# Optimization experiments

Measured on AMD Instinct MI355X. Metric: run time of the kernel, lower is better.

## Reference

```python
import jax, jax.numpy as jnp
import numpy as np

B, K, N, D, L = 16, 16, 1024, 256, 8
LN_EPS = 1e-5


def setup_inputs() -> dict:
    key = jax.random.key(0)
    ks = jax.random.split(key, 12)
    w = lambda k, sh: jax.random.normal(k, sh, jnp.float32) * 0.02
    return {
        "H": jax.random.normal(ks[0], (B, K, N, D), jnp.float32),
        "eps": jax.random.normal(ks[1], (B, L, D), jnp.float32),  # single Gaussian draw per batch
        "mu": jnp.zeros((1, L, D), jnp.float32),
        "log_sigma": jnp.full((1, L, D), -2.0, jnp.float32),
        "Wq": w(ks[2], (D, D)), "bq": jnp.zeros((D,), jnp.float32),
        "Wk": w(ks[3], (D, D)), "bk": jnp.zeros((D,), jnp.float32),
        "Wv": w(ks[4], (D, D)), "bv": jnp.zeros((D,), jnp.float32),
        "W_ih": w(ks[5], (3 * D, D)), "b_ih": jnp.zeros((3 * D,), jnp.float32),
        "W_hh": w(ks[6], (3 * D, D)), "b_hh": jnp.zeros((3 * D,), jnp.float32),
        "W1": w(ks[7], (D, D)), "b1": jnp.zeros((D,), jnp.float32),
        "W2": w(ks[8], (D, D)), "b2": jnp.zeros((D,), jnp.float32),
        "ln_g": jnp.ones((D,), jnp.float32), "ln_b": jnp.zeros((D,), jnp.float32),
    }


def reference(H, eps, mu, log_sigma, Wq, bq, Wk, bk, Wv, bv,
              W_ih, b_ih, W_hh, b_hh, W1, b1, W2, b2, ln_g, ln_b):
    d = H.shape[-1]
    scale = 1.0 / jnp.sqrt(jnp.asarray(d, H.dtype))
    slots0 = mu + jnp.exp(log_sigma) * eps  # [B,L,D]

    def step(slots, h_t):  # slots [B,L,D], h_t [B,N,D]
        Q = slots @ Wq.T + bq
        Kt = h_t @ Wk.T + bk
        V = h_t @ Wv.T + bv
        scores = jnp.einsum("bld,bnd->bln", Q, Kt) * scale
        attn = jnp.nan_to_num(jax.nn.softmax(scores, axis=-1))
        upd = jnp.einsum("bln,bnd->bld", attn, V)
        # torch.nn.GRUCell(input=upd, hidden=slots)
        gi = upd @ W_ih.T + b_ih
        gh = slots @ W_hh.T + b_hh
        ir, iz, inn = jnp.split(gi, 3, axis=-1)
        hr, hz, hn = jnp.split(gh, 3, axis=-1)
        r = jax.nn.sigmoid(ir + hr)
        z = jax.nn.sigmoid(iz + hz)
        n = jnp.tanh(inn + r * hn)
        s2 = (1.0 - z) * n + z * slots
        # FFN + residual + LayerNorm
        ffn = jnp.maximum(s2 @ W1.T + b1, 0.0) @ W2.T + b2
        x = s2 + ffn
        mean = x.mean(axis=-1, keepdims=True)
        var = x.var(axis=-1, keepdims=True)
        s3 = (x - mean) / jnp.sqrt(var + LN_EPS) * ln_g + ln_b
        return s3, (s3, attn)

    _, (S, Beta) = jax.lax.scan(step, slots0, jnp.swapaxes(H, 0, 1))
    return jnp.swapaxes(S, 0, 1), jnp.swapaxes(Beta, 0, 1)  # [B,K,L,D], [B,K,L,N]
```

## Files before the change

### kernel.cpp

```cpp
#include <hip/hip_runtime.h>
#include <math.h>


#define Bn 16
#define KK 16
#define Nn 1024
#define Dn 256
#define Ln 8

#define OFF_WQK   0
#define OFF_BQK   65536
#define OFF_WGIT  65792
#define OFF_BGI   262400
#define OFF_WHHT  263168
#define OFF_W1T   459776
#define OFF_W2T   525312
#define OFF_SLOTS 590848
#define OFF_QK    656384
#define OFF_PAV   689152
#define OFF_PDEN  1737728
#define OFF_PG    1741824
#define OFF_DENS  4887552

__device__ __forceinline__ float sigmoidf_(float x) { return 1.f / (1.f + __expf(-x)); }

__global__ __launch_bounds__(256) void prologue_kernel(
    const float* __restrict__ Wq, const float* __restrict__ bq,
    const float* __restrict__ Wk,
    const float* __restrict__ Wih, const float* __restrict__ bih,
    const float* __restrict__ Wv, const float* __restrict__ bv,
    const float* __restrict__ Whh, const float* __restrict__ W1,
    const float* __restrict__ W2,
    const float* __restrict__ eps, const float* __restrict__ mu,
    const float* __restrict__ lsig,
    float* __restrict__ Wqk, float* __restrict__ bqk,
    float* __restrict__ WgiT, float* __restrict__ bgi,
    float* __restrict__ WhhT, float* __restrict__ W1T, float* __restrict__ W2T,
    float* __restrict__ slots) {
  __shared__ float tile[32][33];
  int wg = blockIdx.x, tid = threadIdx.x;
  if (wg < 257) {
    int w = wg;
    if (w < 256) {
      float acc = 0.f;
#pragma unroll 8
      for (int a = 0; a < 256; ++a) acc += Wq[a * 256 + w] * Wk[a * 256 + tid];
      Wqk[w * 256 + tid] = acc;
    } else {
      float acc = 0.f;
#pragma unroll 8
      for (int a = 0; a < 256; ++a) acc += bq[a] * Wk[a * 256 + tid];
      bqk[tid] = acc;
    }
  } else if (wg < 513) {
    int d = wg - 257;
    float a0 = 0.f, a1 = 0.f, a2 = 0.f;
#pragma unroll 4
    for (int c = 0; c < 256; ++c) {
      float wv = Wv[c * 256 + d];
      a0 += Wih[tid * 256 + c] * wv;
      a1 += Wih[(tid + 256) * 256 + c] * wv;
      a2 += Wih[(tid + 512) * 256 + c] * wv;
    }
    WgiT[d * 768 + tid] = a0;
    WgiT[d * 768 + 256 + tid] = a1;
    WgiT[d * 768 + 512 + tid] = a2;
    if (d < 3) {
      int jj = d * 256 + tid;
      float s = bih[jj];
      for (int c = 0; c < 256; ++c) s += Wih[jj * 256 + c] * bv[c];
      bgi[jj] = s;
    }
  } else if (wg < 833) {
    int sub = wg - 513;
    const float* in; float* out; int R, C, tr, tc;
    if (sub < 192)      { in = Whh; out = WhhT; R = 768; C = 256; tr = sub >> 3; tc = sub & 7; }
    else if (sub < 256) { in = W1;  out = W1T;  R = 256; C = 256; sub -= 192; tr = sub >> 3; tc = sub & 7; }
    else                { in = W2;  out = W2T;  R = 256; C = 256; sub -= 256; tr = sub >> 3; tc = sub & 7; }
    int r = tid >> 5, c = tid & 31;
#pragma unroll
    for (int k = 0; k < 4; ++k)
      tile[r + 8 * k][c] = in[(tr * 32 + r + 8 * k) * C + tc * 32 + c];
    __syncthreads();
#pragma unroll
    for (int k = 0; k < 4; ++k)
      out[(tc * 32 + r + 8 * k) * R + tr * 32 + c] = tile[c][r + 8 * k];
  } else {
    int idx = (wg - 833) * 256 + tid;
    int r = idx & 2047;
    slots[idx] = mu[r] + expf(lsig[r]) * eps[idx];
  }
}

__global__ __launch_bounds__(256) void qk0_kernel(
    const float* __restrict__ Wqk, const float* __restrict__ bqk,
    const float* __restrict__ slots, float* __restrict__ Qkout) {
  __shared__ float sl_s[2048];
  int j = blockIdx.x & 7, b = blockIdx.x >> 3, tid = threadIdx.x;
  for (int k = 0; k < 8; ++k) sl_s[tid + k * 256] = slots[b * 2048 + tid + k * 256];
  __syncthreads();
  int l = tid >> 5, ee = j * 32 + (tid & 31);
  float acc = bqk[ee];
#pragma unroll 8
  for (int d = 0; d < 256; ++d) acc += sl_s[l * 256 + d] * Wqk[d * 256 + ee];
  Qkout[b * 2048 + l * 256 + ee] = acc;
}

__global__ __launch_bounds__(256) void attn_kernel(
    const float* __restrict__ H, const float* __restrict__ Qk,
    float* __restrict__ beta_out, float* __restrict__ par_av,
    float* __restrict__ par_den, int t) {
  __shared__ float h_s[32 * 260];
  __shared__ float qk_s[8 * 260];
  __shared__ float red_a[8 * 256];
  __shared__ float es2[32 * 8];
  __shared__ float red[256];
  int tile = blockIdx.x, b = blockIdx.y, tid = threadIdx.x;
#pragma unroll
  for (int k = 0; k < 8; ++k) {
    int idx = tid + k * 256, l = idx >> 8, e = idx & 255;
    qk_s[l * 260 + e] = Qk[b * 2048 + idx];
  }
  const float4* src = (const float4*)(H + (((long)b * KK + t) * Nn + tile * 32) * Dn);
#pragma unroll
  for (int k = 0; k < 8; ++k) {
    int idx4 = tid + k * 256, r = idx4 >> 6, d4 = idx4 & 63;
    *(float4*)(&h_s[r * 260 + d4 * 4]) = src[idx4];
  }
  __syncthreads();
  {
    int eg = tid >> 5, lh = (tid >> 4) & 1, rq = tid & 15;
    float4 hA[8], hB[8];
    const float4* ha = (const float4*)(&h_s[(rq * 2) * 260 + eg * 32]);
    const float4* hb = (const float4*)(&h_s[(rq * 2 + 1) * 260 + eg * 32]);
#pragma unroll
    for (int i = 0; i < 8; ++i) { hA[i] = ha[i]; hB[i] = hb[i]; }
    float acc[4][2] = {{0.f, 0.f}, {0.f, 0.f}, {0.f, 0.f}, {0.f, 0.f}};
#pragma unroll
    for (int li = 0; li < 4; ++li) {
      const float4* qv = (const float4*)(&qk_s[(lh * 4 + li) * 260 + eg * 32]);
#pragma unroll
      for (int i = 0; i < 8; ++i) {
        float4 qq = qv[i];
        acc[li][0] += qq.x * hA[i].x + qq.y * hA[i].y + qq.z * hA[i].z + qq.w * hA[i].w;
        acc[li][1] += qq.x * hB[i].x + qq.y * hB[i].y + qq.z * hB[i].z + qq.w * hB[i].w;
      }
    }
#pragma unroll
    for (int li = 0; li < 4; ++li) {
      red_a[eg * 256 + (lh * 4 + li) * 32 + rq * 2] = acc[li][0];
      red_a[eg * 256 + (lh * 4 + li) * 32 + rq * 2 + 1] = acc[li][1];
    }
  }
  __syncthreads();
  {
    int l = tid >> 5, row = tid & 31;
    float a = 0.f;
#pragma unroll
    for (int eg = 0; eg < 8; ++eg) a += red_a[eg * 256 + l * 32 + row];
    float ev = __expf(a * 0.0625f);
    es2[row * 8 + l] = ev;
    red[tid] = ev;
    beta_out[(((long)b * KK + t) * Ln + l) * Nn + tile * 32 + row] = ev;
  }
  __syncthreads();
  if (tid < 8) {
    float s = 0.f;
    for (int i = 0; i < 32; ++i) s += red[tid * 32 + i];
    par_den[(b * 32 + tile) * 8 + tid] = s;
  }
  float av[8] = {0.f, 0.f, 0.f, 0.f, 0.f, 0.f, 0.f, 0.f};
  for (int rr = 0; rr < 32; ++rr) {
    float hv = h_s[rr * 260 + tid];
    float4 ea = *(const float4*)(&es2[rr * 8]);
    float4 eb = *(const float4*)(&es2[rr * 8 + 4]);
    av[0] += ea.x * hv; av[1] += ea.y * hv; av[2] += ea.z * hv; av[3] += ea.w * hv;
    av[4] += eb.x * hv; av[5] += eb.y * hv; av[6] += eb.z * hv; av[7] += eb.w * hv;
  }
  long pbase = (long)(b * 32 + tile) * 2048;
#pragma unroll
  for (int i = 0; i < 8; ++i) par_av[pbase + i * 256 + tid] = av[i];
}

__global__ __launch_bounds__(1024) void gru_kernel(
    const float* __restrict__ WgiT, const float* __restrict__ WhhT,
    const float* __restrict__ par_av, const float* __restrict__ par_den,
    const float* __restrict__ slots_cur, float* __restrict__ pg,
    float* __restrict__ dens_all, int t) {
  __shared__ float w_s[16 * 768];
  __shared__ float rupd[8][128];
  __shared__ float x_s[128];
  __shared__ float den_s[8];
  int wid = blockIdx.x;
  int b = wid & 15, kc = (wid >> 4) & 15, role = wid >> 8;
  int tid = threadIdx.x;

  const float* W = role ? (WhhT + kc * 12288) : (WgiT + kc * 12288);
  const float4* wsrc = (const float4*)W;
  float4 wv0 = wsrc[tid], wv1 = wsrc[tid + 1024], wv2 = wsrc[tid + 2048];
  if (role == 0) {
    {
      int g = tid >> 7, le = tid & 127;
      int l = le >> 4, e = le & 15;
      float ps = 0.f;
      long base = ((long)(b * 32)) * 2048 + l * 256 + kc * 16 + e;
#pragma unroll
      for (int i = 0; i < 4; ++i) ps += par_av[base + (long)(g * 4 + i) * 2048];
      rupd[g][le] = ps;
    }
    if (tid < 256) {
      int ll = tid >> 5, tl = tid & 31;
      float dv = par_den[(b * 32 + tl) * 8 + ll];
#pragma unroll
      for (int m = 1; m < 32; m <<= 1) dv += __shfl_xor(dv, m);
      if (tl == 0) den_s[ll] = 1.f / dv;
    }
  } else {
    if (tid < 128) x_s[tid] = slots_cur[b * 2048 + (tid >> 4) * 256 + kc * 16 + (tid & 15)];
  }
  ((float4*)w_s)[tid] = wv0;
  ((float4*)w_s)[tid + 1024] = wv1;
  ((float4*)w_s)[tid + 2048] = wv2;
  __syncthreads();

  if (role == 0) {
    if (kc == 0 && tid < 8) dens_all[(t * 16 + b) * 8 + tid] = den_s[tid];
    if (tid < 128) {
      float s = 0.f;
#pragma unroll
      for (int g = 0; g < 8; ++g) s += rupd[g][tid];
      x_s[tid] = s * den_s[tid >> 4];
    }
    __syncthreads();
  }

  int l4 = tid >> 8, cb = tid & 255;
  int off = role ? 768 : 0;
  long pb0 = ((long)(b * 16 + kc) * 8 + l4) * 1536 + off;
  long pb1 = ((long)(b * 16 + kc) * 8 + l4 + 4) * 1536 + off;
  {
    float a0 = 0.f, a1 = 0.f, a2 = 0.f, a3 = 0.f, a4 = 0.f, a5 = 0.f;
#pragma unroll
    for (int e = 0; e < 16; ++e) {
      float u0 = x_s[l4 * 16 + e];
      float u1 = x_s[(l4 + 4) * 16 + e];
      float w0 = w_s[e * 768 + cb];
      float w1 = w_s[e * 768 + 256 + cb];
      float w2 = w_s[e * 768 + 512 + cb];
      a0 += u0 * w0; a1 += u0 * w1; a2 += u0 * w2;
      a3 += u1 * w0; a4 += u1 * w1; a5 += u1 * w2;
    }
    pg[pb0 + cb] = a0; pg[pb0 + 256 + cb] = a1; pg[pb0 + 512 + cb] = a2;
    pg[pb1 + cb] = a3; pg[pb1 + 256 + cb] = a4; pg[pb1 + 512 + cb] = a5;
  }
}

__global__ __launch_bounds__(1024) void chainm_kernel(
    const float* __restrict__ pg, const float* __restrict__ bgi,
    const float* __restrict__ bhh,
    const float* __restrict__ W1T, const float* __restrict__ b1,
    const float* __restrict__ W2T, const float* __restrict__ b2,
    const float* __restrict__ Wqk, const float* __restrict__ bqk,
    const float* __restrict__ ln_g, const float* __restrict__ ln_b,
    const float* __restrict__ slots_cur, float* __restrict__ slots_nxt,
    float* __restrict__ S, float* __restrict__ QkG, int t) {
  __shared__ float gsum[1536];
  __shared__ float s2_s[256], f1s[256], s3_s[256];
  __shared__ float red4[1024];
  __shared__ float red8[128 * 9];
  __shared__ float lnr[8];
  int wid = blockIdx.x;
  int b = wid & 15, l = (wid >> 4) & 7, ph = wid >> 7;
  int tid = threadIdx.x, q = tid >> 8, c = tid & 255;

  float w1p[16];
  {
    const float* wp = W1T + (q * 64) * 256 + c;
#pragma unroll
    for (int i = 0; i < 16; ++i) w1p[i] = wp[i * 256];
  }

  for (int col = tid; col < 1536; col += 1024) {
    float v[16];
#pragma unroll
    for (int j = 0; j < 16; ++j) v[j] = pg[((long)(b * 16 + j) * 8 + l) * 1536 + col];
    float a = 0.f;
#pragma unroll
    for (int j = 0; j < 16; ++j) a += v[j];
    gsum[col] = a;
  }
  __syncthreads();
  if (tid < 256) {
    float r = sigmoidf_(gsum[c] + bgi[c] + gsum[768 + c] + bhh[c]);
    float z = sigmoidf_(gsum[256 + c] + bgi[256 + c] + gsum[1024 + c] + bhh[256 + c]);
    float n = tanhf(gsum[512 + c] + bgi[512 + c] + r * (gsum[1280 + c] + bhh[512 + c]));
    s2_s[c] = (1.f - z) * n + z * slots_cur[b * 2048 + l * 256 + c];
  }
  __syncthreads();
  {
    const float* wp = W1T + (q * 64) * 256 + c;
    const float* sp = s2_s + q * 64;
    float acc = 0.f;
#pragma unroll
    for (int i = 0; i < 16; ++i) acc += sp[i] * w1p[i];
#pragma unroll
    for (int g = 1; g < 4; ++g) {
      float w[16];
#pragma unroll
      for (int i = 0; i < 16; ++i) w[i] = wp[(g * 16 + i) * 256];
#pragma unroll
      for (int i = 0; i < 16; ++i) acc += sp[g * 16 + i] * w[i];
    }
    red4[q * 256 + c] = acc;
  }
  __syncthreads();
  if (tid < 256)
    f1s[c] = fmaxf(red4[c] + red4[256 + c] + red4[512 + c] + red4[768 + c] + b1[c], 0.f);
  __syncthreads();
  {
    const float* wp = W2T + (q * 64) * 256 + c;
    const float* fp = f1s + q * 64;
    float acc = 0.f;
#pragma unroll
    for (int g = 0; g < 4; ++g) {
      float w[16];
#pragma unroll
      for (int i = 0; i < 16; ++i) w[i] = wp[(g * 16 + i) * 256];
#pragma unroll
      for (int i = 0; i < 16; ++i) acc += fp[g * 16 + i] * w[i];
    }
    red4[q * 256 + c] = acc;
  }
  __syncthreads();
  if (tid < 256) {
    float x = red4[c] + red4[256 + c] + red4[512 + c] + red4[768 + c] + b2[c] + s2_s[c];
    s3_s[c] = x;
    float sr = x, qr = x * x;
#pragma unroll
    for (int m = 1; m < 64; m <<= 1) { sr += __shfl_xor(sr, m); qr += __shfl_xor(qr, m); }
    if ((c & 63) == 0) { lnr[c >> 6] = sr; lnr[4 + (c >> 6)] = qr; }
  }
  __syncthreads();
  if (tid < 256) {
    float m = (lnr[0] + lnr[1] + lnr[2] + lnr[3]) * (1.f / 256.f);
    float v = (lnr[4] + lnr[5] + lnr[6] + lnr[7]) * (1.f / 256.f) - m * m;
    float s3 = (s3_s[c] - m) * rsqrtf(v + 1e-5f) * ln_g[c] + ln_b[c];
    s3_s[c] = s3;
    if (ph == 0) {
      S[(((long)(b * 16) + t) * 8 + l) * 256 + c] = s3;
      slots_nxt[b * 2048 + l * 256 + c] = s3;
    }
  }
  __syncthreads();
  {
    int kc = tid >> 7, cc = tid & 127;
    const float* wp = Wqk + (kc * 32) * 256 + ph * 128 + cc;
    const float* sp = s3_s + kc * 32;
    float acc = 0.f;
#pragma unroll
    for (int g = 0; g < 2; ++g) {
      float w[16];
#pragma unroll
      for (int i = 0; i < 16; ++i) w[i] = wp[(g * 16 + i) * 256];
#pragma unroll
      for (int i = 0; i < 16; ++i) acc += sp[g * 16 + i] * w[i];
    }
    red8[cc * 9 + kc] = acc;
  }
  __syncthreads();
  if (tid < 128) {
    float a = bqk[ph * 128 + tid];
#pragma unroll
    for (int kc = 0; kc < 8; ++kc) a += red8[tid * 9 + kc];
    QkG[b * 2048 + l * 256 + ph * 128 + tid] = a;
  }
}

__global__ __launch_bounds__(1024) void beta_norm_kernel(
    const float* __restrict__ dens_all, float* __restrict__ Beta) {
  int wid = blockIdx.x;
  int b = wid >> 4, t = wid & 15;
  int tid = threadIdx.x;
  long base = (((long)b * 16) + t) * 8192;
#pragma unroll
  for (int i = 0; i < 8; ++i) {
    int idx = i * 1024 + tid;
    int l = idx >> 10;
    Beta[base + idx] *= dens_all[(t * 16 + b) * 8 + l];
  }
}

extern "C" void kernel_launch(void* const* d_in, const int* in_sizes, int n_in,
                              void* d_out, int out_size, void* d_ws, size_t ws_size,
                              hipStream_t stream) {
  const float* H    = (const float*)d_in[0];
  const float* eps  = (const float*)d_in[1];
  const float* mu   = (const float*)d_in[2];
  const float* lsig = (const float*)d_in[3];
  const float* Wq   = (const float*)d_in[4];
  const float* bq   = (const float*)d_in[5];
  const float* Wk   = (const float*)d_in[6];
  const float* Wv   = (const float*)d_in[8];
  const float* bv   = (const float*)d_in[9];
  const float* Wih  = (const float*)d_in[10];
  const float* bih  = (const float*)d_in[11];
  const float* Whh  = (const float*)d_in[12];
  const float* bhh  = (const float*)d_in[13];
  const float* W1   = (const float*)d_in[14];
  const float* b1   = (const float*)d_in[15];
  const float* W2   = (const float*)d_in[16];
  const float* b2   = (const float*)d_in[17];
  const float* ln_g = (const float*)d_in[18];
  const float* ln_b = (const float*)d_in[19];

  float* out = (float*)d_out;
  float* S    = out;
  float* Beta = out + (long)Bn * KK * Ln * Dn;

  float* ws = (float*)d_ws;
  float* Wqk    = ws + OFF_WQK;
  float* bqk    = ws + OFF_BQK;
  float* WgiT   = ws + OFF_WGIT;
  float* bgi    = ws + OFF_BGI;
  float* WhhT   = ws + OFF_WHHT;
  float* W1T    = ws + OFF_W1T;
  float* W2T    = ws + OFF_W2T;
  float* slots0 = ws + OFF_SLOTS;
  float* Qk     = ws + OFF_QK;
  float* pav    = ws + OFF_PAV;
  float* pden   = ws + OFF_PDEN;
  float* pg     = ws + OFF_PG;
  float* dens   = ws + OFF_DENS;

  prologue_kernel<<<961, 256, 0, stream>>>(Wq, bq, Wk, Wih, bih, Wv, bv, Whh, W1, W2,
                                           eps, mu, lsig,
                                           Wqk, bqk, WgiT, bgi, WhhT, W1T, W2T, slots0);
  qk0_kernel<<<128, 256, 0, stream>>>(Wqk, bqk, slots0, Qk);

  for (int t = 0; t < KK; ++t) {
    float* scur = slots0 + (t & 1) * 32768;
    float* snxt = slots0 + ((t + 1) & 1) * 32768;
    attn_kernel<<<dim3(32, 16), 256, 0, stream>>>(H, Qk, Beta, pav, pden, t);
    gru_kernel<<<512, 1024, 0, stream>>>(WgiT, WhhT, pav, pden, scur, pg, dens, t);
    chainm_kernel<<<256, 1024, 0, stream>>>(pg, bgi, bhh, W1T, b1, W2T, b2,
                                            Wqk, bqk, ln_g, ln_b, scur, snxt,
                                            S, Qk, t);
  }
  beta_norm_kernel<<<256, 1024, 0, stream>>>(dens, Beta);
}
```

Measured before the change: 880.6 us.

## Replace partial-sum buffers with atomic accumulation into double-buffered reducers

The attention, GRU and gate reductions now add their partial sums directly into small per-batch accumulators with atomic adds, instead of writing full partial buffers that the next kernel reads back and sums. The accumulators are double-buffered across timesteps, are zeroed once in the prologue, and the chain kernel zeroes the next step's buffers. This removes several MB of partial-buffer traffic and the reduction loops. In exchange it adds atomic contention and makes summation order nondeterministic.

```diff
diff --git a/kernel.cpp b/kernel.cpp
--- a/kernel.cpp
+++ b/kernel.cpp
@@ -17,10 +17,9 @@
 #define OFF_W2T   525312
 #define OFF_SLOTS 590848
 #define OFF_QK    656384
-#define OFF_PAV   689152
-#define OFF_PDEN  1737728
-#define OFF_PG    1741824
-#define OFF_DENS  4887552
+#define OFF_ACC   689152
+#define ACC_STRIDE 229504
+#define OFF_DENS  1148160
 
 __device__ __forceinline__ float sigmoidf_(float x) { return 1.f / (1.f + __expf(-x)); }
 
@@ -36,7 +35,7 @@
     float* __restrict__ Wqk, float* __restrict__ bqk,
     float* __restrict__ WgiT, float* __restrict__ bgi,
     float* __restrict__ WhhT, float* __restrict__ W1T, float* __restrict__ W2T,
-    float* __restrict__ slots) {
+    float* __restrict__ slots, float* __restrict__ acc0) {
   __shared__ float tile[32][33];
   int wg = blockIdx.x, tid = threadIdx.x;
   if (wg < 257) {
@@ -85,10 +84,13 @@
 #pragma unroll
     for (int k = 0; k < 4; ++k)
       out[(tc * 32 + r + 8 * k) * R + tr * 32 + c] = tile[c][r + 8 * k];
-  } else {
+  } else if (wg < 961) {
     int idx = (wg - 833) * 256 + tid;
     int r = idx & 2047;
     slots[idx] = mu[r] + expf(lsig[r]) * eps[idx];
+  } else {
+    int idx = (wg - 961) * 256 + tid;
+    if (idx < ACC_STRIDE) acc0[idx] = 0.f;
   }
 }
 
@@ -108,8 +110,8 @@
 
 __global__ __launch_bounds__(256) void attn_kernel(
     const float* __restrict__ H, const float* __restrict__ Qk,
-    float* __restrict__ beta_out, float* __restrict__ par_av,
-    float* __restrict__ par_den, int t) {
+    float* __restrict__ beta_out, float* __restrict__ updr,
+    float* __restrict__ denr, int t) {
   __shared__ float h_s[32 * 260];
   __shared__ float qk_s[8 * 260];
   __shared__ float red_a[8 * 256];
@@ -167,7 +169,7 @@
   if (tid < 8) {
     float s = 0.f;
     for (int i = 0; i < 32; ++i) s += red[tid * 32 + i];
-    par_den[(b * 32 + tile) * 8 + tid] = s;
+    unsafeAtomicAdd(&denr[b * 8 + tid], s);
   }
   float av[8] = {0.f, 0.f, 0.f, 0.f, 0.f, 0.f, 0.f, 0.f};
   for (int rr = 0; rr < 32; ++rr) {
@@ -177,44 +179,31 @@
     av[0] += ea.x * hv; av[1] += ea.y * hv; av[2] += ea.z * hv; av[3] += ea.w * hv;
     av[4] += eb.x * hv; av[5] += eb.y * hv; av[6] += eb.z * hv; av[7] += eb.w * hv;
   }
-  long pbase = (long)(b * 32 + tile) * 2048;
-#pragma unroll
-  for (int i = 0; i < 8; ++i) par_av[pbase + i * 256 + tid] = av[i];
+#pragma unroll
+  for (int i = 0; i < 8; ++i)
+    unsafeAtomicAdd(&updr[b * 2048 + i * 256 + tid], av[i]);
 }
 
 __global__ __launch_bounds__(1024) void gru_kernel(
     const float* __restrict__ WgiT, const float* __restrict__ WhhT,
-    const float* __restrict__ par_av, const float* __restrict__ par_den,
-    const float* __restrict__ slots_cur, float* __restrict__ pg,
+    const float* __restrict__ updr, const float* __restrict__ denr,
+    const float* __restrict__ slots_cur, float* __restrict__ gsum,
     float* __restrict__ dens_all, int t) {
   __shared__ float w_s[16 * 768];
-  __shared__ float rupd[8][128];
   __shared__ float x_s[128];
-  __shared__ float den_s[8];
   int wid = blockIdx.x;
   int b = wid & 15, kc = (wid >> 4) & 15, role = wid >> 8;
   int tid = threadIdx.x;
 
-  const float* W = role ? (WhhT + kc * 12288) : (WgiT + kc * 12288);
-  const float4* wsrc = (const float4*)W;
+  const float4* wsrc = (const float4*)((role ? WhhT : WgiT) + kc * 12288);
   float4 wv0 = wsrc[tid], wv1 = wsrc[tid + 1024], wv2 = wsrc[tid + 2048];
   if (role == 0) {
-    {
-      int g = tid >> 7, le = tid & 127;
-      int l = le >> 4, e = le & 15;
-      float ps = 0.f;
-      long base = ((long)(b * 32)) * 2048 + l * 256 + kc * 16 + e;
-#pragma unroll
-      for (int i = 0; i < 4; ++i) ps += par_av[base + (long)(g * 4 + i) * 2048];
-      rupd[g][le] = ps;
-    }
-    if (tid < 256) {
-      int ll = tid >> 5, tl = tid & 31;
-      float dv = par_den[(b * 32 + tl) * 8 + ll];
-#pragma unroll
-      for (int m = 1; m < 32; m <<= 1) dv += __shfl_xor(dv, m);
-      if (tl == 0) den_s[ll] = 1.f / dv;
-    }
+    if (tid < 128) {
+      int l = tid >> 4, e = tid & 15;
+      float rd = 1.f / denr[b * 8 + l];
+      x_s[tid] = updr[b * 2048 + l * 256 + kc * 16 + e] * rd;
+    }
+    if (kc == 0 && tid < 8) dens_all[(t * 16 + b) * 8 + tid] = 1.f / denr[b * 8 + tid];
   } else {
     if (tid < 128) x_s[tid] = slots_cur[b * 2048 + (tid >> 4) * 256 + kc * 16 + (tid & 15)];
   }
@@ -223,48 +212,39 @@
   ((float4*)w_s)[tid + 2048] = wv2;
   __syncthreads();
 
-  if (role == 0) {
-    if (kc == 0 && tid < 8) dens_all[(t * 16 + b) * 8 + tid] = den_s[tid];
-    if (tid < 128) {
-      float s = 0.f;
-#pragma unroll
-      for (int g = 0; g < 8; ++g) s += rupd[g][tid];
-      x_s[tid] = s * den_s[tid >> 4];
-    }
-    __syncthreads();
-  }
-
   int l4 = tid >> 8, cb = tid & 255;
   int off = role ? 768 : 0;
-  long pb0 = ((long)(b * 16 + kc) * 8 + l4) * 1536 + off;
-  long pb1 = ((long)(b * 16 + kc) * 8 + l4 + 4) * 1536 + off;
-  {
-    float a0 = 0.f, a1 = 0.f, a2 = 0.f, a3 = 0.f, a4 = 0.f, a5 = 0.f;
-#pragma unroll
-    for (int e = 0; e < 16; ++e) {
-      float u0 = x_s[l4 * 16 + e];
-      float u1 = x_s[(l4 + 4) * 16 + e];
-      float w0 = w_s[e * 768 + cb];
-      float w1 = w_s[e * 768 + 256 + cb];
-      float w2 = w_s[e * 768 + 512 + cb];
-      a0 += u0 * w0; a1 += u0 * w1; a2 += u0 * w2;
-      a3 += u1 * w0; a4 += u1 * w1; a5 += u1 * w2;
-    }
-    pg[pb0 + cb] = a0; pg[pb0 + 256 + cb] = a1; pg[pb0 + 512 + cb] = a2;
-    pg[pb1 + cb] = a3; pg[pb1 + 256 + cb] = a4; pg[pb1 + 512 + cb] = a5;
-  }
+  float a0 = 0.f, a1 = 0.f, a2 = 0.f, a3 = 0.f, a4 = 0.f, a5 = 0.f;
+#pragma unroll
+  for (int e = 0; e < 16; ++e) {
+    float u0 = x_s[l4 * 16 + e];
+    float u1 = x_s[(l4 + 4) * 16 + e];
+    float w0 = w_s[e * 768 + cb];
+    float w1 = w_s[e * 768 + 256 + cb];
+    float w2 = w_s[e * 768 + 512 + cb];
+    a0 += u0 * w0; a1 += u0 * w1; a2 += u0 * w2;
+    a3 += u1 * w0; a4 += u1 * w1; a5 += u1 * w2;
+  }
+  float* g0 = gsum + (b * 8 + l4) * 1536 + off;
+  float* g1 = gsum + (b * 8 + l4 + 4) * 1536 + off;
+  unsafeAtomicAdd(g0 + cb, a0);
+  unsafeAtomicAdd(g0 + 256 + cb, a1);
+  unsafeAtomicAdd(g0 + 512 + cb, a2);
+  unsafeAtomicAdd(g1 + cb, a3);
+  unsafeAtomicAdd(g1 + 256 + cb, a4);
+  unsafeAtomicAdd(g1 + 512 + cb, a5);
 }
 
 __global__ __launch_bounds__(1024) void chainm_kernel(
-    const float* __restrict__ pg, const float* __restrict__ bgi,
-    const float* __restrict__ bhh,
+    const float* __restrict__ gsum_c, float* __restrict__ updr_n,
+    float* __restrict__ denr_n, float* __restrict__ gsum_n,
+    const float* __restrict__ bgi, const float* __restrict__ bhh,
     const float* __restrict__ W1T, const float* __restrict__ b1,
     const float* __restrict__ W2T, const float* __restrict__ b2,
     const float* __restrict__ Wqk, const float* __restrict__ bqk,
     const float* __restrict__ ln_g, const float* __restrict__ ln_b,
     const float* __restrict__ slots_cur, float* __restrict__ slots_nxt,
     float* __restrict__ S, float* __restrict__ QkG, int t) {
-  __shared__ float gsum[1536];
   __shared__ float s2_s[256], f1s[256], s3_s[256];
   __shared__ float red4[1024];
   __shared__ float red8[128 * 9];
@@ -280,23 +260,23 @@
     for (int i = 0; i < 16; ++i) w1p[i] = wp[i * 256];
   }
 
-  for (int col = tid; col < 1536; col += 1024) {
-    float v[16];
-#pragma unroll
-    for (int j = 0; j < 16; ++j) v[j] = pg[((long)(b * 16 + j) * 8 + l) * 1536 + col];
-    float a = 0.f;
-#pragma unroll
-    for (int j = 0; j < 16; ++j) a += v[j];
-    gsum[col] = a;
-  }
-  __syncthreads();
   if (tid < 256) {
-    float r = sigmoidf_(gsum[c] + bgi[c] + gsum[768 + c] + bhh[c]);
-    float z = sigmoidf_(gsum[256 + c] + bgi[256 + c] + gsum[1024 + c] + bhh[256 + c]);
-    float n = tanhf(gsum[512 + c] + bgi[512 + c] + r * (gsum[1280 + c] + bhh[512 + c]));
+    const float* gs = gsum_c + (b * 8 + l) * 1536;
+    float gir = gs[c], giz = gs[256 + c], gin = gs[512 + c];
+    float ghr = gs[768 + c], ghz = gs[1024 + c], ghn = gs[1280 + c];
+    float r = sigmoidf_(gir + bgi[c] + ghr + bhh[c]);
+    float z = sigmoidf_(giz + bgi[256 + c] + ghz + bhh[256 + c]);
+    float n = tanhf(gin + bgi[512 + c] + r * (ghn + bhh[512 + c]));
     s2_s[c] = (1.f - z) * n + z * slots_cur[b * 2048 + l * 256 + c];
   }
   __syncthreads();
+  if (ph == 0) {
+    float* gz = gsum_n + (b * 8 + l) * 1536;
+    gz[tid] = 0.f;
+    if (tid < 512) gz[1024 + tid] = 0.f;
+    if (tid < 256) updr_n[b * 2048 + l * 256 + tid] = 0.f;
+    if (tid == 0) denr_n[b * 8 + l] = 0.f;
+  }
   {
     const float* wp = W1T + (q * 64) * 256 + c;
     const float* sp = s2_s + q * 64;
@@ -427,22 +407,28 @@
   float* W2T    = ws + OFF_W2T;
   float* slots0 = ws + OFF_SLOTS;
   float* Qk     = ws + OFF_QK;
-  float* pav    = ws + OFF_PAV;
-  float* pden   = ws + OFF_PDEN;
-  float* pg     = ws + OFF_PG;
+  float* acc    = ws + OFF_ACC;
   float* dens   = ws + OFF_DENS;
 
-  prologue_kernel<<<961, 256, 0, stream>>>(Wq, bq, Wk, Wih, bih, Wv, bv, Whh, W1, W2,
-                                           eps, mu, lsig,
-                                           Wqk, bqk, WgiT, bgi, WhhT, W1T, W2T, slots0);
+  prologue_kernel<<<1858, 256, 0, stream>>>(Wq, bq, Wk, Wih, bih, Wv, bv, Whh, W1, W2,
+                                            eps, mu, lsig,
+                                            Wqk, bqk, WgiT, bgi, WhhT, W1T, W2T,
+                                            slots0, acc);
   qk0_kernel<<<128, 256, 0, stream>>>(Wqk, bqk, slots0, Qk);
 
   for (int t = 0; t < KK; ++t) {
     float* scur = slots0 + (t & 1) * 32768;
     float* snxt = slots0 + ((t + 1) & 1) * 32768;
-    attn_kernel<<<dim3(32, 16), 256, 0, stream>>>(H, Qk, Beta, pav, pden, t);
-    gru_kernel<<<512, 1024, 0, stream>>>(WgiT, WhhT, pav, pden, scur, pg, dens, t);
-    chainm_kernel<<<256, 1024, 0, stream>>>(pg, bgi, bhh, W1T, b1, W2T, b2,
+    float* accc = acc + (t & 1) * ACC_STRIDE;
+    float* accn = acc + ((t + 1) & 1) * ACC_STRIDE;
+    float* updr_c = accc;             float* updr_n = accn;
+    float* denr_c = accc + 32768;     float* denr_n = accn + 32768;
+    float* gsum_c = accc + 32896;     float* gsum_n = accn + 32896;
+    attn_kernel<<<dim3(32, 16), 256, 0, stream>>>(H, Qk, Beta, updr_c, denr_c, t);
+    gru_kernel<<<512, 1024, 0, stream>>>(WgiT, WhhT, updr_c, denr_c, scur,
+                                         gsum_c, dens, t);
+    chainm_kernel<<<256, 1024, 0, stream>>>(gsum_c, updr_n, denr_n, gsum_n,
+                                            bgi, bhh, W1T, b1, W2T, b2,
                                             Wqk, bqk, ln_g, ln_b, scur, snxt,
                                             S, Qk, t);
   }
```

New measurement: 959.0 us. 8.9% more time.
